# Performance work log

Hardware: AMD Instinct MI355X
Metric: run time of the kernel (lower is better)

Reference implementation:

```python
import jax, jax.numpy as jnp
import numpy as np
import math

D_MODEL = 1024
N_HEADS = 16
B, L, K = 2, 512, 4


def sinusoidal_pe(n, dim):
    # matches SinusoidalEmbedding buffer pe[:n]
    position = jnp.arange(n, dtype=jnp.float32)[:, None]
    div_term = jnp.exp(jnp.arange(0, dim, 2, dtype=jnp.float32) * (-math.log(10000.0) / dim))
    ang = position * div_term  # [n, dim//2]
    pe = jnp.zeros((n, dim), dtype=jnp.float32)
    pe = pe.at[:, 0::2].set(jnp.sin(ang))
    pe = pe.at[:, 1::2].set(jnp.cos(ang))
    return pe


def setup_inputs() -> dict:
    key = jax.random.key(0)
    ks = jax.random.split(key, 8)
    s = 1.0 / math.sqrt(D_MODEL)
    return {
        "h": jax.random.normal(ks[0], (B, L, K, D_MODEL), dtype=jnp.float32),
        "probs": jax.random.uniform(ks[1], (B, L, K), dtype=jnp.float32),
        "Wq": jax.random.normal(ks[2], (D_MODEL, D_MODEL), dtype=jnp.float32) * s,
        "bq": jnp.zeros((D_MODEL,), dtype=jnp.float32),
        "Wk": jax.random.normal(ks[3], (D_MODEL, D_MODEL), dtype=jnp.float32) * s,
        "bk": jnp.zeros((D_MODEL,), dtype=jnp.float32),
        "Wv": jax.random.normal(ks[4], (D_MODEL, D_MODEL), dtype=jnp.float32) * s,
        "bv": jnp.zeros((D_MODEL,), dtype=jnp.float32),
        "Wo": jax.random.normal(ks[5], (D_MODEL, D_MODEL), dtype=jnp.float32) * s,
        "bo": jnp.zeros((D_MODEL,), dtype=jnp.float32),
        "prob_bias_scale": jnp.float32(1.0),
        "n_heads": N_HEADS,
    }


def reference(h, probs, Wq, bq, Wk, bk, Wv, bv, Wo, bo, prob_bias_scale, n_heads):
    Bh, Lh, kh, D = h.shape
    N = Lh * kh
    hd = D // n_heads
    scale = hd ** (-0.5)

    h_flat = h.reshape(Bh, N, D) + sinusoidal_pe(N, D)[None]  # [B, N, D]
    probs_flat = probs.reshape(Bh, N)

    # torch Linear: x @ W.T + b
    q = (h_flat @ Wq.T + bq).reshape(Bh, N, n_heads, hd).transpose(0, 2, 1, 3)
    key = (h_flat @ Wk.T + bk).reshape(Bh, N, n_heads, hd).transpose(0, 2, 1, 3)
    v = (h_flat @ Wv.T + bv).reshape(Bh, N, n_heads, hd).transpose(0, 2, 1, 3)

    scores = jnp.einsum("bhnd,bhmd->bhnm", q, key) * scale  # [B,H,N,N]
    prob_bias = jnp.log(probs_flat + 1e-8)[:, None, None, :]  # bias on key axis
    scores = scores + prob_bias_scale * prob_bias
    attn = jax.nn.softmax(scores, axis=-1)  # dropout is identity in eval
    out = jnp.einsum("bhnm,bhmd->bhnd", attn, v)
    out = out.transpose(0, 2, 1, 3).reshape(Bh, N, D)
    out = out @ Wo.T + bo
    return out.reshape(Bh, Lh, kh, D)
```

## Files before the change

kernel.cpp:

```cpp
#include <hip/hip_runtime.h>

typedef _Float16 h8 __attribute__((ext_vector_type(8)));
typedef _Float16 h4 __attribute__((ext_vector_type(4)));
typedef __fp16 fp16x2 __attribute__((ext_vector_type(2)));
typedef float f32x4 __attribute__((ext_vector_type(4)));

#define NSEQ 2048
#define DMODEL 1024
#define HD 64
#define C2 0.1803368801111244f

#define OFF_HPE  (size_t)0
#define OFF_WQ   (size_t)8388608
#define OFF_WK   (size_t)10485760
#define OFF_WV   (size_t)12582912
#define OFF_WO   (size_t)14680064
#define OFF_Q    (size_t)16777216
#define OFF_K    (size_t)25165824
#define OFF_VT   (size_t)33554432
#define OFF_AO   (size_t)41943040
#define OFF_PB   (size_t)50331648

#define GLL(g, l) __builtin_amdgcn_global_load_lds( \
    (const __attribute__((address_space(1))) unsigned int*)(const void*)(g), \
    (__attribute__((address_space(3))) unsigned int*)(l), 16, 0, 0)

__global__ void prep_kernel(const float* __restrict__ h, _Float16* __restrict__ hpe,
                            const float* __restrict__ w0, const float* __restrict__ w1,
                            const float* __restrict__ w2, const float* __restrict__ w3,
                            _Float16* __restrict__ d0, _Float16* __restrict__ d1,
                            _Float16* __restrict__ d2, _Float16* __restrict__ d3,
                            const float* __restrict__ probs, const float* __restrict__ pbs,
                            float* __restrict__ pb) {
    int idx = blockIdx.x * blockDim.x + threadIdx.x;
    if (idx < 524288) {
        int row = idx >> 7;
        int c8 = (idx & 127) * 8;
        int n = row & (NSEQ - 1);
        const float kL = -0.025952563241307517f;
        const float kInv2Pi = 0.15915494309189535f;
        union { float4 f4[2]; float f[8]; } in;
        in.f4[0] = *(const float4*)&h[(size_t)row * DMODEL + c8];
        in.f4[1] = *(const float4*)&h[(size_t)row * DMODEL + c8 + 4];
        union { _Float16 hh[8]; uint4 u; } out;
        #pragma unroll
        for (int p = 0; p < 4; ++p) {
            int i2 = (c8 >> 1) + p;
            float div = __builtin_amdgcn_exp2f((float)i2 * kL);
            float rev = (float)n * div * kInv2Pi;
            float rf = __builtin_amdgcn_fractf(rev);
            float s = __builtin_amdgcn_sinf(rf);
            float c = __builtin_amdgcn_cosf(rf);
            out.hh[2 * p]     = (_Float16)(in.f[2 * p] + s);
            out.hh[2 * p + 1] = (_Float16)(in.f[2 * p + 1] + c);
        }
        *(uint4*)&hpe[(size_t)row * DMODEL + c8] = out.u;
    } else if (idx < 1572864) {
        int j = idx - 524288;
        int which = j >> 18, i2 = j & 262143;
        const float* s = which == 0 ? w0 : which == 1 ? w1 : which == 2 ? w2 : w3;
        _Float16* d    = which == 0 ? d0 : which == 1 ? d1 : which == 2 ? d2 : d3;
        float sc = which == 0 ? C2 : 1.0f;
        float4 v = ((const float4*)s)[i2];
        union { _Float16 hh[4]; uint2 u; } o;
        o.hh[0] = (_Float16)(v.x * sc); o.hh[1] = (_Float16)(v.y * sc);
        o.hh[2] = (_Float16)(v.z * sc); o.hh[3] = (_Float16)(v.w * sc);
        ((uint2*)d)[i2] = o.u;
    } else if (idx < 1576960) {
        int k = idx - 1572864;
        pb[k] = pbs[0] * log2f(probs[k] + 1e-8f);
    }
}

__global__ __launch_bounds__(512) void gemm_qkv(
    const _Float16* __restrict__ A,
    const _Float16* __restrict__ Wqp, const _Float16* __restrict__ Wkp, const _Float16* __restrict__ Wvp,
    const float* __restrict__ bqp, const float* __restrict__ bkp, const float* __restrict__ bvp,
    _Float16* __restrict__ qb, _Float16* __restrict__ kb, _Float16* __restrict__ vt)
{
    __shared__ __align__(16) _Float16 As[256][64];
    __shared__ __align__(16) _Float16 Bs[128][64];
    int bid = blockIdx.x;
    int nf = (bid & 7) * 48 + (bid >> 3);
    int bx = nf & 15, byy = nf >> 4;
    int widx = byy >> 3;
    const _Float16* W = widx == 0 ? Wqp : widx == 1 ? Wkp : Wvp;
    const float* bias = widx == 0 ? bqp : widx == 1 ? bkp : bvp;
    float bscale = widx == 0 ? C2 : 1.0f;
    int tm = bx * 256;
    int tn = (byy & 7) * 128;
    int t = threadIdx.x;
    int wave = t >> 6, lane = t & 63;
    int wr = (wave >> 1) * 64, wc = (wave & 1) * 64;
    int lr = lane & 15, lg = lane >> 4;

    f32x4 acc[4][4] = {};

    int grow = lane >> 3;
    int gcol = (lane & 7) * 8;
    const _Float16* Aptr = A + (size_t)(tm + wave * 8 + grow) * DMODEL + gcol;
    const _Float16* Wptr = W + (size_t)(tn + wave * 8 + grow) * DMODEL + gcol;

    for (int k0 = 0; k0 < DMODEL; k0 += 64) {
        __syncthreads();
        #pragma unroll
        for (int i = 0; i < 4; ++i)
            GLL(Aptr + (size_t)i * 64 * DMODEL + k0, &As[i * 64 + wave * 8][0]);
        #pragma unroll
        for (int i = 0; i < 2; ++i)
            GLL(Wptr + (size_t)i * 64 * DMODEL + k0, &Bs[i * 64 + wave * 8][0]);
        __syncthreads();
        #pragma unroll
        for (int kk = 0; kk < 2; ++kk) {
            h8 af[4], bf[4];
            #pragma unroll
            for (int mi = 0; mi < 4; ++mi) af[mi] = *(const h8*)&As[wr + mi * 16 + lr][kk * 32 + lg * 8];
            #pragma unroll
            for (int ni = 0; ni < 4; ++ni) bf[ni] = *(const h8*)&Bs[wc + ni * 16 + lr][kk * 32 + lg * 8];
            #pragma unroll
            for (int mi = 0; mi < 4; ++mi)
                #pragma unroll
                for (int ni = 0; ni < 4; ++ni)
                    acc[mi][ni] = __builtin_amdgcn_mfma_f32_16x16x32_f16(af[mi], bf[ni], acc[mi][ni], 0, 0, 0);
        }
    }

    #pragma unroll
    for (int mi = 0; mi < 4; ++mi)
        #pragma unroll
        for (int ni = 0; ni < 4; ++ni) {
            int col = tn + wc + ni * 16 + lr;
            float bv = bias[col] * bscale;
            if (widx < 2) {
                _Float16* dst = widx == 0 ? qb : kb;
                #pragma unroll
                for (int j = 0; j < 4; ++j) {
                    int row = tm + wr + mi * 16 + lg * 4 + j;
                    dst[(size_t)row * DMODEL + col] = (_Float16)(acc[mi][ni][j] + bv);
                }
            } else {
                int row0 = tm + wr + mi * 16 + lg * 4;
                int b = row0 >> 11, n0 = row0 & 2047;
                h4 pk;
                #pragma unroll
                for (int j = 0; j < 4; ++j) pk[j] = (_Float16)(acc[mi][ni][j] + bv);
                *(h4*)&vt[((size_t)b * 1024 + col) * 2048 + n0] = pk;
            }
        }
}

__global__ __launch_bounds__(256) void gemm_ao(
    const _Float16* __restrict__ A, const _Float16* __restrict__ W,
    const float* __restrict__ bias, float* __restrict__ C)
{
    __shared__ __align__(16) _Float16 As[64][64];
    __shared__ __align__(16) _Float16 Bs[128][64];
    int bid = blockIdx.x + 64 * blockIdx.y;
    int nf = (bid & 7) * 64 + (bid >> 3);
    int tm = (nf & 63) * 64;
    int tn = (nf >> 6) * 128;
    int t = threadIdx.x;
    int wave = t >> 6, lane = t & 63;
    int wr = (wave >> 1) * 32, wc = (wave & 1) * 64;
    int lr = lane & 15, lg = lane >> 4;

    f32x4 acc[2][4] = {};

    int grow = lane >> 3;
    int gcol = (lane & 7) * 8;
    const _Float16* Aptr = A + (size_t)(tm + wave * 8 + grow) * DMODEL + gcol;
    const _Float16* Wptr = W + (size_t)(tn + wave * 8 + grow) * DMODEL + gcol;

    for (int k0 = 0; k0 < DMODEL; k0 += 64) {
        __syncthreads();
        #pragma unroll
        for (int i = 0; i < 2; ++i)
            GLL(Aptr + (size_t)i * 32 * DMODEL + k0, &As[i * 32 + wave * 8][0]);
        #pragma unroll
        for (int i = 0; i < 4; ++i)
            GLL(Wptr + (size_t)i * 32 * DMODEL + k0, &Bs[i * 32 + wave * 8][0]);
        __syncthreads();
        #pragma unroll
        for (int kk = 0; kk < 2; ++kk) {
            h8 af[2], bf[4];
            #pragma unroll
            for (int mi = 0; mi < 2; ++mi) af[mi] = *(const h8*)&As[wr + mi * 16 + lr][kk * 32 + lg * 8];
            #pragma unroll
            for (int ni = 0; ni < 4; ++ni) bf[ni] = *(const h8*)&Bs[wc + ni * 16 + lr][kk * 32 + lg * 8];
            #pragma unroll
            for (int mi = 0; mi < 2; ++mi)
                #pragma unroll
                for (int ni = 0; ni < 4; ++ni)
                    acc[mi][ni] = __builtin_amdgcn_mfma_f32_16x16x32_f16(af[mi], bf[ni], acc[mi][ni], 0, 0, 0);
        }
    }

    #pragma unroll
    for (int mi = 0; mi < 2; ++mi)
        #pragma unroll
        for (int ni = 0; ni < 4; ++ni)
            #pragma unroll
            for (int j = 0; j < 4; ++j) {
                int row = tm + wr + mi * 16 + lg * 4 + j;
                int col = tn + wc + ni * 16 + lr;
                C[(size_t)row * DMODEL + col] = acc[mi][ni][j] + bias[col];
            }
}

#define KT 64

#define SWZ(row, bytecol) ((row) * 128 + ((bytecol) ^ (((row) & 7) << 4)))

__global__ __launch_bounds__(512) void flash_kernel(
    const _Float16* __restrict__ Qb,
    const _Float16* __restrict__ Kb,
    const _Float16* __restrict__ Vt,
    const float* __restrict__ pb,
    _Float16* __restrict__ AO)
{
    __shared__ __align__(16) char KsB[2][8192];
    __shared__ __align__(16) char VsB[2][8192];
    __shared__ __align__(16) _Float16 Ps[8][16][72];

    int bid = blockIdx.x + 16 * blockIdx.y;
    int nf = (bid & 7) * 64 + (bid >> 3);
    int qx = nf & 15, bh = nf >> 4;
    int b = bh >> 4, h = bh & 15;
    int q0 = qx * 128;
    int t = threadIdx.x, wave = t >> 6, lane = t & 63;
    int lr = lane & 15, lg = lane >> 4;

    const _Float16* Khead  = Kb + (size_t)b * NSEQ * DMODEL + h * HD;
    const _Float16* Vthead = Vt + ((size_t)b * 1024 + h * HD) * NSEQ;
    const float* pbb = pb + b * NSEQ;

    const _Float16* Qrow = Qb + ((size_t)b * NSEQ + q0 + wave * 16 + lr) * DMODEL + h * HD;
    h8 qf0 = *(const h8*)&Qrow[lg * 8];
    h8 qf1 = *(const h8*)&Qrow[32 + lg * 8];

    const h8 vones = { (_Float16)1, (_Float16)1, (_Float16)1, (_Float16)1,
                       (_Float16)1, (_Float16)1, (_Float16)1, (_Float16)1 };

    float mrun = -INFINITY;
    f32x4 oacc[4] = {};
    f32x4 lsum = {};

    int srow = t >> 3;
    int schunk = (t & 7) ^ (srow & 7);
    const _Float16* Ksrc = Khead + (size_t)srow * DMODEL + schunk * 8;
    const _Float16* Vsrc = Vthead + (size_t)srow * NSEQ + schunk * 8;

    GLL(Ksrc, KsB[0] + wave * 1024);
    GLL(Vsrc, VsB[0] + wave * 1024);
    asm volatile("s_waitcnt vmcnt(0)" ::: "memory");
    __syncthreads();

    int cur = 0;
    for (int kt = 0; kt < 32; ++kt) {
        int k0 = kt * KT;
        if (kt < 31) {
            GLL(Ksrc + (size_t)(k0 + KT) * DMODEL, KsB[cur ^ 1] + wave * 1024);
            GLL(Vsrc + (k0 + KT), VsB[cur ^ 1] + wave * 1024);
        }
        const char* Kc = KsB[cur];
        const char* Vc = VsB[cur];

        f32x4 s[4];
        #pragma unroll
        for (int ci = 0; ci < 4; ++ci)
            s[ci] = *(const f32x4*)&pbb[k0 + ci * 16 + lg * 4];
        __builtin_amdgcn_s_setprio(1);
        #pragma unroll
        for (int ci = 0; ci < 4; ++ci) {
            h8 kf = *(const h8*)(Kc + SWZ(ci * 16 + lr, lg * 16));
            s[ci] = __builtin_amdgcn_mfma_f32_16x16x32_f16(kf, qf0, s[ci], 0, 0, 0);
        }
        #pragma unroll
        for (int ci = 0; ci < 4; ++ci) {
            h8 kf = *(const h8*)(Kc + SWZ(ci * 16 + lr, 64 + lg * 16));
            s[ci] = __builtin_amdgcn_mfma_f32_16x16x32_f16(kf, qf1, s[ci], 0, 0, 0);
        }
        __builtin_amdgcn_s_setprio(0);

        h8 vf[2][4];
        #pragma unroll
        for (int kb = 0; kb < 2; ++kb)
            #pragma unroll
            for (int ni = 0; ni < 4; ++ni)
                vf[kb][ni] = *(const h8*)(Vc + SWZ(ni * 16 + lr, kb * 64 + lg * 16));

        asm volatile("s_waitcnt vmcnt(0) lgkmcnt(0)" ::: "memory");
        __syncthreads();
        cur ^= 1;

        float sm = s[0][0];
        #pragma unroll
        for (int ci = 0; ci < 4; ++ci)
            #pragma unroll
            for (int j = 0; j < 4; ++j) sm = fmaxf(sm, s[ci][j]);
        sm = fmaxf(sm, __shfl_xor(sm, 16));
        sm = fmaxf(sm, __shfl_xor(sm, 32));

        bool need = __any(sm > mrun);
        float newm = need ? fmaxf(mrun, sm) : mrun;

        #pragma unroll
        for (int ci = 0; ci < 4; ++ci) {
            fp16x2 a = __builtin_amdgcn_cvt_pkrtz(__builtin_amdgcn_exp2f(s[ci][0] - newm),
                                                  __builtin_amdgcn_exp2f(s[ci][1] - newm));
            fp16x2 b2 = __builtin_amdgcn_cvt_pkrtz(__builtin_amdgcn_exp2f(s[ci][2] - newm),
                                                   __builtin_amdgcn_exp2f(s[ci][3] - newm));
            union { fp16x2 hh[2]; uint2 u; } pk;
            pk.hh[0] = a; pk.hh[1] = b2;
            *(uint2*)&Ps[wave][lr][ci * 16 + lg * 4] = pk.u;
        }

        if (need) {
            float fs = __builtin_amdgcn_exp2f(mrun - newm);
            mrun = newm;
            #pragma unroll
            for (int j = 0; j < 4; ++j) {
                float fsj = __shfl(fs, (lane & 48) | (lg * 4 + j), 64);
                #pragma unroll
                for (int ni = 0; ni < 4; ++ni) oacc[ni][j] *= fsj;
                lsum[j] *= fsj;
            }
        }

        asm volatile("s_waitcnt lgkmcnt(0)" ::: "memory");
        __builtin_amdgcn_sched_barrier(0);

        __builtin_amdgcn_s_setprio(1);
        #pragma unroll
        for (int kb = 0; kb < 2; ++kb) {
            h8 pa = *(const h8*)&Ps[wave][lr][kb * 32 + lg * 8];
            #pragma unroll
            for (int ni = 0; ni < 4; ++ni)
                oacc[ni] = __builtin_amdgcn_mfma_f32_16x16x32_f16(pa, vf[kb][ni], oacc[ni], 0, 0, 0);
            lsum = __builtin_amdgcn_mfma_f32_16x16x32_f16(pa, vones, lsum, 0, 0, 0);
        }
        __builtin_amdgcn_s_setprio(0);
    }

    #pragma unroll
    for (int j = 0; j < 4; ++j) {
        float inv = 1.0f / lsum[j];
        int row = q0 + wave * 16 + lg * 4 + j;
        #pragma unroll
        for (int ni = 0; ni < 4; ++ni)
            AO[((size_t)b * NSEQ + row) * DMODEL + h * HD + ni * 16 + lr] = (_Float16)(oacc[ni][j] * inv);
    }
}

extern "C" void kernel_launch(void* const* d_in, const int* in_sizes, int n_in,
                              void* d_out, int out_size, void* d_ws, size_t ws_size,
                              hipStream_t stream) {
    const float* h    = (const float*)d_in[0];
    const float* prob = (const float*)d_in[1];
    const float* Wq   = (const float*)d_in[2];
    const float* bq   = (const float*)d_in[3];
    const float* Wk   = (const float*)d_in[4];
    const float* bk   = (const float*)d_in[5];
    const float* Wv   = (const float*)d_in[6];
    const float* bv   = (const float*)d_in[7];
    const float* Wo   = (const float*)d_in[8];
    const float* bo   = (const float*)d_in[9];
    const float* pbs  = (const float*)d_in[10];

    char* ws = (char*)d_ws;
    _Float16* hpe  = (_Float16*)(ws + OFF_HPE);
    _Float16* wq16 = (_Float16*)(ws + OFF_WQ);
    _Float16* wk16 = (_Float16*)(ws + OFF_WK);
    _Float16* wv16 = (_Float16*)(ws + OFF_WV);
    _Float16* wo16 = (_Float16*)(ws + OFF_WO);
    _Float16* qb   = (_Float16*)(ws + OFF_Q);
    _Float16* kb16 = (_Float16*)(ws + OFF_K);
    _Float16* vt   = (_Float16*)(ws + OFF_VT);
    _Float16* ao   = (_Float16*)(ws + OFF_AO);
    float*    pbuf = (float*)(ws + OFF_PB);

    prep_kernel<<<dim3(6160), dim3(256), 0, stream>>>(
        h, hpe, Wq, Wk, Wv, Wo, wq16, wk16, wv16, wo16, prob, pbs, pbuf);

    gemm_qkv<<<dim3(384), dim3(512), 0, stream>>>(hpe, wq16, wk16, wv16, bq, bk, bv, qb, kb16, vt);

    flash_kernel<<<dim3(16, 32), dim3(512), 0, stream>>>(qb, kb16, vt, pbuf, ao);

    gemm_ao<<<dim3(64, 8), dim3(256), 0, stream>>>(ao, wo16, bo, (float*)d_out);
}
```

Baseline: 218.8 us.

## Double-buffer LDS in QKV and output GEMMs, shrink QKV tile to 128x128

Both projection GEMMs now use two LDS buffers and prefetch the next K-slice with global_load_lds while MFMAs run on the current one. This leaves one barrier per iteration instead of two and hides global load latency. The QKV GEMM tile also shrinks from 256x128 with 512 threads to 128x128 with 256 threads, doubling the grid to 768 blocks for better CU coverage. In exchange, LDS use per block doubles and A-tile reuse per block drops.

```diff
diff --git a/kernel.cpp b/kernel.cpp
--- a/kernel.cpp
+++ b/kernel.cpp
@@ -72,22 +72,22 @@
     }
 }
 
-__global__ __launch_bounds__(512) void gemm_qkv(
+__global__ __launch_bounds__(256) void gemm_qkv(
     const _Float16* __restrict__ A,
     const _Float16* __restrict__ Wqp, const _Float16* __restrict__ Wkp, const _Float16* __restrict__ Wvp,
     const float* __restrict__ bqp, const float* __restrict__ bkp, const float* __restrict__ bvp,
     _Float16* __restrict__ qb, _Float16* __restrict__ kb, _Float16* __restrict__ vt)
 {
-    __shared__ __align__(16) _Float16 As[256][64];
-    __shared__ __align__(16) _Float16 Bs[128][64];
+    __shared__ __align__(16) _Float16 As[2][128][64];
+    __shared__ __align__(16) _Float16 Bs[2][128][64];
     int bid = blockIdx.x;
-    int nf = (bid & 7) * 48 + (bid >> 3);
-    int bx = nf & 15, byy = nf >> 4;
+    int nf = (bid & 7) * 96 + (bid >> 3);
+    int bx = nf & 31, byy = nf >> 5;
     int widx = byy >> 3;
     const _Float16* W = widx == 0 ? Wqp : widx == 1 ? Wkp : Wvp;
     const float* bias = widx == 0 ? bqp : widx == 1 ? bkp : bvp;
     float bscale = widx == 0 ? C2 : 1.0f;
-    int tm = bx * 256;
+    int tm = bx * 128;
     int tn = (byy & 7) * 128;
     int t = threadIdx.x;
     int wave = t >> 6, lane = t & 63;
@@ -101,28 +101,38 @@
     const _Float16* Aptr = A + (size_t)(tm + wave * 8 + grow) * DMODEL + gcol;
     const _Float16* Wptr = W + (size_t)(tn + wave * 8 + grow) * DMODEL + gcol;
 
-    for (int k0 = 0; k0 < DMODEL; k0 += 64) {
-        __syncthreads();
+    auto STAGE = [&](int buf, int k0) {
         #pragma unroll
         for (int i = 0; i < 4; ++i)
-            GLL(Aptr + (size_t)i * 64 * DMODEL + k0, &As[i * 64 + wave * 8][0]);
-        #pragma unroll
-        for (int i = 0; i < 2; ++i)
-            GLL(Wptr + (size_t)i * 64 * DMODEL + k0, &Bs[i * 64 + wave * 8][0]);
-        __syncthreads();
+            GLL(Aptr + (size_t)i * 32 * DMODEL + k0, &As[buf][i * 32 + wave * 8][0]);
+        #pragma unroll
+        for (int i = 0; i < 4; ++i)
+            GLL(Wptr + (size_t)i * 32 * DMODEL + k0, &Bs[buf][i * 32 + wave * 8][0]);
+    };
+
+    STAGE(0, 0);
+    asm volatile("s_waitcnt vmcnt(0)" ::: "memory");
+    __syncthreads();
+
+    int cur = 0;
+    for (int kt = 0; kt < 16; ++kt) {
+        if (kt < 15) STAGE(cur ^ 1, (kt + 1) * 64);
         #pragma unroll
         for (int kk = 0; kk < 2; ++kk) {
             h8 af[4], bf[4];
             #pragma unroll
-            for (int mi = 0; mi < 4; ++mi) af[mi] = *(const h8*)&As[wr + mi * 16 + lr][kk * 32 + lg * 8];
-            #pragma unroll
-            for (int ni = 0; ni < 4; ++ni) bf[ni] = *(const h8*)&Bs[wc + ni * 16 + lr][kk * 32 + lg * 8];
+            for (int mi = 0; mi < 4; ++mi) af[mi] = *(const h8*)&As[cur][wr + mi * 16 + lr][kk * 32 + lg * 8];
+            #pragma unroll
+            for (int ni = 0; ni < 4; ++ni) bf[ni] = *(const h8*)&Bs[cur][wc + ni * 16 + lr][kk * 32 + lg * 8];
             #pragma unroll
             for (int mi = 0; mi < 4; ++mi)
                 #pragma unroll
                 for (int ni = 0; ni < 4; ++ni)
                     acc[mi][ni] = __builtin_amdgcn_mfma_f32_16x16x32_f16(af[mi], bf[ni], acc[mi][ni], 0, 0, 0);
         }
+        asm volatile("s_waitcnt vmcnt(0) lgkmcnt(0)" ::: "memory");
+        __syncthreads();
+        cur ^= 1;
     }
 
     #pragma unroll
@@ -153,9 +163,9 @@
     const _Float16* __restrict__ A, const _Float16* __restrict__ W,
     const float* __restrict__ bias, float* __restrict__ C)
 {
-    __shared__ __align__(16) _Float16 As[64][64];
-    __shared__ __align__(16) _Float16 Bs[128][64];
-    int bid = blockIdx.x + 64 * blockIdx.y;
+    __shared__ __align__(16) _Float16 As[2][64][64];
+    __shared__ __align__(16) _Float16 Bs[2][128][64];
+    int bid = blockIdx.x;
     int nf = (bid & 7) * 64 + (bid >> 3);
     int tm = (nf & 63) * 64;
     int tn = (nf >> 6) * 128;
@@ -171,28 +181,38 @@
     const _Float16* Aptr = A + (size_t)(tm + wave * 8 + grow) * DMODEL + gcol;
     const _Float16* Wptr = W + (size_t)(tn + wave * 8 + grow) * DMODEL + gcol;
 
-    for (int k0 = 0; k0 < DMODEL; k0 += 64) {
-        __syncthreads();
+    auto STAGE = [&](int buf, int k0) {
         #pragma unroll
         for (int i = 0; i < 2; ++i)
-            GLL(Aptr + (size_t)i * 32 * DMODEL + k0, &As[i * 32 + wave * 8][0]);
+            GLL(Aptr + (size_t)i * 32 * DMODEL + k0, &As[buf][i * 32 + wave * 8][0]);
         #pragma unroll
         for (int i = 0; i < 4; ++i)
-            GLL(Wptr + (size_t)i * 32 * DMODEL + k0, &Bs[i * 32 + wave * 8][0]);
-        __syncthreads();
+            GLL(Wptr + (size_t)i * 32 * DMODEL + k0, &Bs[buf][i * 32 + wave * 8][0]);
+    };
+
+    STAGE(0, 0);
+    asm volatile("s_waitcnt vmcnt(0)" ::: "memory");
+    __syncthreads();
+
+    int cur = 0;
+    for (int kt = 0; kt < 16; ++kt) {
+        if (kt < 15) STAGE(cur ^ 1, (kt + 1) * 64);
         #pragma unroll
         for (int kk = 0; kk < 2; ++kk) {
             h8 af[2], bf[4];
             #pragma unroll
-            for (int mi = 0; mi < 2; ++mi) af[mi] = *(const h8*)&As[wr + mi * 16 + lr][kk * 32 + lg * 8];
-            #pragma unroll
-            for (int ni = 0; ni < 4; ++ni) bf[ni] = *(const h8*)&Bs[wc + ni * 16 + lr][kk * 32 + lg * 8];
+            for (int mi = 0; mi < 2; ++mi) af[mi] = *(const h8*)&As[cur][wr + mi * 16 + lr][kk * 32 + lg * 8];
+            #pragma unroll
+            for (int ni = 0; ni < 4; ++ni) bf[ni] = *(const h8*)&Bs[cur][wc + ni * 16 + lr][kk * 32 + lg * 8];
             #pragma unroll
             for (int mi = 0; mi < 2; ++mi)
                 #pragma unroll
                 for (int ni = 0; ni < 4; ++ni)
                     acc[mi][ni] = __builtin_amdgcn_mfma_f32_16x16x32_f16(af[mi], bf[ni], acc[mi][ni], 0, 0, 0);
         }
+        asm volatile("s_waitcnt vmcnt(0) lgkmcnt(0)" ::: "memory");
+        __syncthreads();
+        cur ^= 1;
     }
 
     #pragma unroll
@@ -382,9 +402,9 @@
     prep_kernel<<<dim3(6160), dim3(256), 0, stream>>>(
         h, hpe, Wq, Wk, Wv, Wo, wq16, wk16, wv16, wo16, prob, pbs, pbuf);
 
-    gemm_qkv<<<dim3(384), dim3(512), 0, stream>>>(hpe, wq16, wk16, wv16, bq, bk, bv, qb, kb16, vt);
+    gemm_qkv<<<dim3(768), dim3(256), 0, stream>>>(hpe, wq16, wk16, wv16, bq, bk, bv, qb, kb16, vt);
 
     flash_kernel<<<dim3(16, 32), dim3(512), 0, stream>>>(qb, kb16, vt, pbuf, ao);
 
-    gemm_ao<<<dim3(64, 8), dim3(256), 0, stream>>>(ao, wo16, bo, (float*)d_out);
+    gemm_ao<<<dim3(512), dim3(256), 0, stream>>>(ao, wo16, bo, (float*)d_out);
 }
```

Result: slower. 236.0 us (+7.9%).
